# Kernel tuning notes

Hardware: AMD Instinct MI355X
Metric: run time of the kernel (lower is better)

## Reference

```python
import jax, jax.numpy as jnp
import numpy as np

B, T, F = 1024, 512, 32
H, E, L = 128, 16, 2
N_TICKERS = 5000


def _gru_layer(x_seq, W_ih, W_hh, b_ih, b_hh):
    # x_seq: [B, T, I]; W_ih: [3H, I]; W_hh: [3H, H]. PyTorch gate order: r, z, n.
    gx = jnp.einsum('bti,gi->btg', x_seq, W_ih) + b_ih  # [B, T, 3H]

    def step(h, gx_t):
        gh = h @ W_hh.T + b_hh                     # [B, 3H]
        r = jax.nn.sigmoid(gx_t[:, :H] + gh[:, :H])
        z = jax.nn.sigmoid(gx_t[:, H:2 * H] + gh[:, H:2 * H])
        n = jnp.tanh(gx_t[:, 2 * H:] + r * gh[:, 2 * H:])
        h_new = (1.0 - z) * n + z * h
        return h_new, h_new

    h0 = jnp.zeros((x_seq.shape[0], H), dtype=x_seq.dtype)
    _, hs = jax.lax.scan(step, h0, jnp.swapaxes(gx, 0, 1))  # hs: [T, B, H]
    return jnp.swapaxes(hs, 0, 1)                            # [B, T, H]


def setup_inputs() -> dict:
    key = jax.random.key(0)
    ks = jax.random.split(key, 16)
    s_in0 = 1.0 / np.sqrt(H)
    inp = {
        'x': jax.random.normal(ks[0], (B, T, F), dtype=jnp.float32),
        'ticker_ids': jax.random.randint(ks[1], (B,), 0, N_TICKERS),
        'embed': jax.random.normal(ks[2], (N_TICKERS, E), dtype=jnp.float32),
        # GRU layer 0 (input size F+E=48)
        'W_ih0': jax.random.uniform(ks[3], (3 * H, F + E), minval=-s_in0, maxval=s_in0),
        'W_hh0': jax.random.uniform(ks[4], (3 * H, H), minval=-s_in0, maxval=s_in0),
        'b_ih0': jax.random.uniform(ks[5], (3 * H,), minval=-s_in0, maxval=s_in0),
        'b_hh0': jax.random.uniform(ks[6], (3 * H,), minval=-s_in0, maxval=s_in0),
        # GRU layer 1 (input size H)
        'W_ih1': jax.random.uniform(ks[7], (3 * H, H), minval=-s_in0, maxval=s_in0),
        'W_hh1': jax.random.uniform(ks[8], (3 * H, H), minval=-s_in0, maxval=s_in0),
        'b_ih1': jax.random.uniform(ks[9], (3 * H,), minval=-s_in0, maxval=s_in0),
        'b_hh1': jax.random.uniform(ks[10], (3 * H,), minval=-s_in0, maxval=s_in0),
        # head: Linear(H,H) -> ReLU -> Linear(H,1)
        'head_w1': jax.random.uniform(ks[11], (H, H), minval=-s_in0, maxval=s_in0),
        'head_b1': jax.random.uniform(ks[12], (H,), minval=-s_in0, maxval=s_in0),
        'head_w2': jax.random.uniform(ks[13], (1, H), minval=-s_in0, maxval=s_in0),
        'head_b2': jax.random.uniform(ks[14], (1,), minval=-s_in0, maxval=s_in0),
    }
    return inp


def reference(x, ticker_ids, embed, W_ih0, W_hh0, b_ih0, b_hh0,
              W_ih1, W_hh1, b_ih1, b_hh1, head_w1, head_b1, head_w2, head_b2):
    emb = embed[ticker_ids]                                  # [B, E]
    emb_seq = jnp.broadcast_to(emb[:, None, :], (x.shape[0], x.shape[1], emb.shape[-1]))
    xcat = jnp.concatenate([x, emb_seq], axis=-1)            # [B, T, F+E]
    h = _gru_layer(xcat, W_ih0, W_hh0, b_ih0, b_hh0)         # [B, T, H]
    h = _gru_layer(h, W_ih1, W_hh1, b_ih1, b_hh1)            # [B, T, H]
    last = h[:, -1, :]                                       # [B, H]
    hid = jax.nn.relu(last @ head_w1.T + head_b1)            # dropout inactive at eval
    y = (hid @ head_w2.T + head_b2)[:, 0]                    # [B]
    return y
```

## Files before the change

### kernel.cpp

```cpp
#include <hip/hip_runtime.h>

constexpr int kB  = 1024;
constexpr int kT  = 512;
constexpr int kF  = 32;
constexpr int kE  = 16;
constexpr int kH  = 128;
constexpr int kMB = 16;
constexpr int kNMB = kB / kMB;
constexpr int kTc = 32;
constexpr int kNCh = kT / kTc;
constexpr int kTg = kTc / 2;
constexpr size_t kH0Str = (size_t)kB * kTc * kH;
constexpr size_t kSlots = (size_t)kNMB * kTc * 512;
constexpr size_t kGx0Str = kSlots * 12;

typedef __attribute__((ext_vector_type(8))) _Float16 f16x8;
typedef __attribute__((ext_vector_type(4))) _Float16 f16x4;
typedef __attribute__((ext_vector_type(4))) float    f32x4;

#define MFMA16(a,b,c) __builtin_amdgcn_mfma_f32_16x16x32_f16(a,b,c,0,0,0)

__device__ __forceinline__ float sigm_hw(float x){
    float e = __builtin_amdgcn_exp2f(-1.442695041f * x);
    return __builtin_amdgcn_rcpf(1.0f + e);
}
__device__ __forceinline__ float tanh_hw(float x){
    float e = __builtin_amdgcn_exp2f(-2.885390082f * x);
    return fmaf(2.0f, __builtin_amdgcn_rcpf(1.0f + e), -1.0f);
}
__device__ __forceinline__ void splitF(float v, _Float16 &hi, _Float16 &lo){
    hi = (_Float16)v;
    lo = (_Float16)(v - (float)hi);
}
__device__ __forceinline__ f16x8 loadW8(const float* __restrict__ p){
    f16x8 r;
#pragma unroll
    for (int j=0;j<8;j++) r[j] = (_Float16)p[j];
    return r;
}
__device__ __forceinline__ unsigned short f2u(_Float16 h){ return __builtin_bit_cast(unsigned short, h); }
__device__ __forceinline__ _Float16 u2f(unsigned short u){ return __builtin_bit_cast(_Float16, u); }
__device__ __forceinline__ unsigned pack2(float a, float b){
    return (unsigned)f2u((_Float16)a) | ((unsigned)f2u((_Float16)b) << 16);
}
__device__ __forceinline__ float uf(unsigned u){ return __builtin_bit_cast(float, u); }
__device__ __forceinline__ void bar_lds(){
    asm volatile("s_waitcnt lgkmcnt(0)\n\ts_barrier" ::: "memory");
}

struct SRec {
    alignas(16) _Float16 hH[2][16][136];
    alignas(16) _Float16 hL[2][16][136];
    alignas(16) float hf[16][132];
    alignas(16) float hf2[16][132];
};
struct SGem {
    alignas(16) _Float16 aH[2][16][136];
    alignas(16) _Float16 aL[2][16][136];
};
union SU { SRec r; SGem g; };

__attribute__((amdgpu_waves_per_eu(2, 2)))
__global__ void __launch_bounds__(512) rnn_fused(
    const float* __restrict__ x, const int* __restrict__ tick,
    const float* __restrict__ embed,
    const float* __restrict__ Wih0, const float* __restrict__ Whh0,
    const float* __restrict__ bih0, const float* __restrict__ bhh0,
    const float* __restrict__ Wih1, const float* __restrict__ bih1,
    const float* __restrict__ Whh1, const float* __restrict__ bhh1,
    const float* __restrict__ hw1, const float* __restrict__ hb1,
    const float* __restrict__ hw2, const float* __restrict__ hb2,
    unsigned* __restrict__ h0seq, unsigned* __restrict__ gxA,
    unsigned* __restrict__ gxB, float* __restrict__ h1state,
    unsigned* __restrict__ gx0, float* __restrict__ out, int c)
{
    __shared__ SU sm;
    const int tid = threadIdx.x;
    const int w = tid >> 6, l = tid & 63, lm = l & 15, lq = l >> 4;
    const int i = 16*w + lm;
    const int cls[3] = { i, 128 + i, 256 + i };

    if (blockIdx.x < 64) {
        if (c < 0 || c >= kNCh) return;
        SRec &S = sm.r;
        const int mb = blockIdx.x, b0 = mb * kMB;
        unsigned* h0w = h0seq + (size_t)(c & 1) * kH0Str;
        const unsigned* g0 = gx0 + (size_t)(c & 1) * kGx0Str;

        f16x8 wv[3][4];
#pragma unroll
        for (int T=0; T<3; T++)
#pragma unroll
            for (int kt=0; kt<4; kt++)
                wv[T][kt] = loadW8(Whh0 + (size_t)cls[T]*kH + kt*32 + lq*8);
        const float br = bhh0[cls[0]], bz = bhh0[cls[1]], bn = bhh0[cls[2]];

        float hreg[4];
        if (c == 0){
#pragma unroll
            for (int q=0;q<4;q++){
                hreg[q]=0.f;
                S.hH[0][lq*4+q][i]=(_Float16)0.f;
                S.hL[0][lq*4+q][i]=(_Float16)0.f;
            }
        } else {
            const unsigned* h0p = h0seq + (size_t)((c-1) & 1) * kH0Str;
#pragma unroll
            for (int q=0;q<4;q++){
                unsigned u = h0p[((size_t)(mb*kTc + kTc-1)*16 + lq*4+q)*kH + i];
                _Float16 hh = u2f((unsigned short)(u>>16)), hl = u2f((unsigned short)u);
                hreg[q] = (float)hh + (float)hl;
                S.hH[0][lq*4+q][i]=hh; S.hL[0][lq*4+q][i]=hl;
            }
        }
        const size_t base = (size_t)mb*kTc*512 + tid;
        uint4 grc = *(const uint4*)(g0 + base*12);
        uint4 gzc = *(const uint4*)(g0 + base*12 + 4);
        uint4 gnc = *(const uint4*)(g0 + base*12 + 8);
        uint4 grn = *(const uint4*)(g0 + (base+512)*12);
        uint4 gzn = *(const uint4*)(g0 + (base+512)*12 + 4);
        uint4 gnn = *(const uint4*)(g0 + (base+512)*12 + 8);
        bar_lds();

        int buf = 0;
        for (int tc=0; tc<kTc; tc++){
            const int nb = buf ^ 1;
            f16x8 aHf[4], aLf[4];
#pragma unroll
            for (int kt=0;kt<4;kt++){
                aHf[kt] = *(const f16x8*)&S.hH[buf][lm][kt*32 + lq*8];
                aLf[kt] = *(const f16x8*)&S.hL[buf][lm][kt*32 + lq*8];
            }
            f32x4 aR={br,br,br,br}, aZ={bz,bz,bz,bz}, aNH={bn,bn,bn,bn};
#pragma unroll
            for (int kt=0;kt<4;kt++){
                aR =MFMA16(aHf[kt],wv[0][kt],aR);  aR =MFMA16(aLf[kt],wv[0][kt],aR);
                aZ =MFMA16(aHf[kt],wv[1][kt],aZ);  aZ =MFMA16(aLf[kt],wv[1][kt],aZ);
                aNH=MFMA16(aHf[kt],wv[2][kt],aNH); aNH=MFMA16(aLf[kt],wv[2][kt],aNH);
            }
            const float rx[4] = { uf(grc.x), uf(grc.y), uf(grc.z), uf(grc.w) };
            const float zx[4] = { uf(gzc.x), uf(gzc.y), uf(gzc.z), uf(gzc.w) };
            const float nx[4] = { uf(gnc.x), uf(gnc.y), uf(gnc.z), uf(gnc.w) };
            unsigned pk[4];
#pragma unroll
            for (int q=0;q<4;q++){
                float r = sigm_hw(aR[q] + rx[q]);
                float z = sigm_hw(aZ[q] + zx[q]);
                float n = tanh_hw(fmaf(r, aNH[q], nx[q]));
                float h = fmaf(z, hreg[q]-n, n);
                hreg[q] = h;
                _Float16 hh,hl; splitF(h,hh,hl);
                S.hH[nb][lq*4+q][i]=hh;
                S.hL[nb][lq*4+q][i]=hl;
                pk[q] = ((unsigned)f2u(hh)<<16) | f2u(hl);
            }
#pragma unroll
            for (int q=0;q<4;q++)
                h0w[((size_t)(mb*kTc + tc)*16 + lq*4+q)*kH + i] = pk[q];
            grc = grn; gzc = gzn; gnc = gnn;
            int tn = tc + 2; if (tn > kTc-1) tn = kTc-1;
            grn = *(const uint4*)(g0 + (base + (size_t)tn*512)*12);
            gzn = *(const uint4*)(g0 + (base + (size_t)tn*512)*12 + 4);
            gnn = *(const uint4*)(g0 + (base + (size_t)tn*512)*12 + 8);
            bar_lds();
            buf = nb;
        }
    } else if (blockIdx.x < 192) {
        const int bid = blockIdx.x - 64;
        const int mb = bid >> 1, t0 = (bid & 1) * kTg;
        const int b0 = mb * kMB;
        const int g = c - 1;
        if (g >= 0 && g < kNCh) {
            SGem &S = sm.g;
            const unsigned* h0r = h0seq + (size_t)(g & 1) * kH0Str;
            unsigned* gA = gxA + (size_t)(g & 1) * kSlots * 4;
            unsigned* gB = gxB + (size_t)(g & 1) * kSlots * 2;

            f16x8 wv[3][4]; float bI[3];
#pragma unroll
            for (int T=0; T<3; T++){
#pragma unroll
                for (int kt=0; kt<4; kt++)
                    wv[T][kt] = loadW8(Wih1 + (size_t)cls[T]*kH + kt*32 + lq*8);
                bI[T] = bih1[cls[T]];
            }
            const int sr = tid >> 5, sq = tid & 31;
            auto ld = [&](int t){
                return *(const uint4*)(h0r + ((size_t)(mb*kTc + t)*16 + sr)*kH + 4*sq);
            };
            auto stage = [&](int bf, uint4 u){
                f16x4 vh = { u2f((unsigned short)(u.x>>16)), u2f((unsigned short)(u.y>>16)),
                             u2f((unsigned short)(u.z>>16)), u2f((unsigned short)(u.w>>16)) };
                f16x4 vl = { u2f((unsigned short)u.x), u2f((unsigned short)u.y),
                             u2f((unsigned short)u.z), u2f((unsigned short)u.w) };
                *(f16x4*)&S.aH[bf][sr][4*sq] = vh;
                *(f16x4*)&S.aL[bf][sr][4*sq] = vl;
            };
            stage(0, ld(t0));
            uint4 nxt = ld(t0 + 1);
            bar_lds();
            for (int tt=0; tt<kTg; tt++){
                const int t = t0 + tt, bf = tt & 1;
                f16x8 fH[4], fL[4];
#pragma unroll
                for (int kt=0;kt<4;kt++){
                    fH[kt] = *(const f16x8*)&S.aH[bf][lm][kt*32 + lq*8];
                    fL[kt] = *(const f16x8*)&S.aL[bf][lm][kt*32 + lq*8];
                }
                if (tt+1 < kTg) stage(bf^1, nxt);
                if (tt+2 < kTg) nxt = ld(t0 + tt + 2);
                f32x4 aR = {bI[0],bI[0],bI[0],bI[0]};
                f32x4 aZ = {bI[1],bI[1],bI[1],bI[1]};
                f32x4 aN = {bI[2],bI[2],bI[2],bI[2]};
#pragma unroll
                for (int kt=0;kt<4;kt++){
                    aR=MFMA16(fH[kt],wv[0][kt],aR); aR=MFMA16(fL[kt],wv[0][kt],aR);
                    aZ=MFMA16(fH[kt],wv[1][kt],aZ); aZ=MFMA16(fL[kt],wv[1][kt],aZ);
                    aN=MFMA16(fH[kt],wv[2][kt],aN); aN=MFMA16(fL[kt],wv[2][kt],aN);
                }
                const size_t slot = ((size_t)mb*kTc + t)*512 + tid;
                *(uint4*)(gA + slot*4) = make_uint4(pack2(aR[0],aR[1]), pack2(aR[2],aR[3]),
                                                    pack2(aZ[0],aZ[1]), pack2(aZ[2],aZ[3]));
                *(uint2*)(gB + slot*2) = make_uint2(pack2(aN[0],aN[1]), pack2(aN[2],aN[3]));
                bar_lds();
            }
        }
        const int p = c + 1;
        if (p >= 0 && p < kNCh) {
            unsigned* g0w = gx0 + (size_t)(p & 1) * kGx0Str;
            f16x8 xw[3];
#pragma unroll
            for (int T=0; T<3; T++)
                xw[T] = loadW8(Wih0 + (size_t)cls[T]*48 + lq*8);
            float ini[3][4];
            {
                const float bi0 = bih0[cls[0]], bi1 = bih0[cls[1]], bi2 = bih0[cls[2]];
                const float* w0 = Wih0 + (size_t)cls[0]*48 + 32;
                const float* w1 = Wih0 + (size_t)cls[1]*48 + 32;
                const float* w2 = Wih0 + (size_t)cls[2]*48 + 32;
#pragma unroll
                for (int q=0; q<4; q++){
                    const float* ep = embed + (size_t)tick[b0 + lq*4 + q] * kE;
                    float s0=0.f, s1=0.f, s2=0.f;
#pragma unroll
                    for (int e=0; e<kE; e++){
                        float ev = ep[e];
                        s0 = fmaf(ev, w0[e], s0);
                        s1 = fmaf(ev, w1[e], s1);
                        s2 = fmaf(ev, w2[e], s2);
                    }
                    ini[0][q]=bi0+s0; ini[1][q]=bi1+s1; ini[2][q]=bi2+s2;
                }
            }
            for (int tt=0; tt<kTg; tt++){
                const int t = t0 + tt;
                const float* xp = x + (size_t)(b0+lm)*kT*kF + (size_t)(p*kTc + t)*kF + lq*8;
                const float4 xa = *(const float4*)xp;
                const float4 xb = *(const float4*)(xp + 4);
                const float xv[8] = { xa.x, xa.y, xa.z, xa.w, xb.x, xb.y, xb.z, xb.w };
                f16x8 xH, xL;
#pragma unroll
                for (int j=0;j<8;j++){
                    _Float16 hh,hl; splitF(xv[j],hh,hl);
                    xH[j]=hh; xL[j]=hl;
                }
                f32x4 aR = {ini[0][0],ini[0][1],ini[0][2],ini[0][3]};
                f32x4 aZ = {ini[1][0],ini[1][1],ini[1][2],ini[1][3]};
                f32x4 aN = {ini[2][0],ini[2][1],ini[2][2],ini[2][3]};
                aR=MFMA16(xH,xw[0],aR); aR=MFMA16(xL,xw[0],aR);
                aZ=MFMA16(xH,xw[1],aZ); aZ=MFMA16(xL,xw[1],aZ);
                aN=MFMA16(xH,xw[2],aN); aN=MFMA16(xL,xw[2],aN);
                const size_t slot = ((size_t)mb*kTc + t)*512 + tid;
                *(uint4*)(g0w + slot*12)     = __builtin_bit_cast(uint4, aR);
                *(uint4*)(g0w + slot*12 + 4) = __builtin_bit_cast(uint4, aZ);
                *(uint4*)(g0w + slot*12 + 8) = __builtin_bit_cast(uint4, aN);
            }
        }
    } else {
        const int e0 = c - 2;
        if (e0 < 0 || e0 >= kNCh) return;
        SRec &S = sm.r;
        const int mb = blockIdx.x - 192, b0 = mb * kMB;
        const unsigned* gA = gxA + (size_t)(e0 & 1) * kSlots * 4;
        const unsigned* gB = gxB + (size_t)(e0 & 1) * kSlots * 2;

        f16x8 wv[3][4];
#pragma unroll
        for (int T=0; T<3; T++)
#pragma unroll
            for (int kt=0; kt<4; kt++)
                wv[T][kt] = loadW8(Whh1 + (size_t)cls[T]*kH + kt*32 + lq*8);
        const float br = bhh1[cls[0]], bz = bhh1[cls[1]], bn = bhh1[cls[2]];

        float hreg[4];
        if (e0 == 0){
#pragma unroll
            for (int q=0;q<4;q++){
                hreg[q]=0.f;
                S.hH[0][lq*4+q][i]=(_Float16)0.f;
                S.hL[0][lq*4+q][i]=(_Float16)0.f;
            }
        } else {
#pragma unroll
            for (int q=0;q<4;q++){
                float h = h1state[(size_t)(b0 + lq*4+q)*kH + i];
                hreg[q]=h;
                _Float16 hh,hl; splitF(h,hh,hl);
                S.hH[0][lq*4+q][i]=hh; S.hL[0][lq*4+q][i]=hl;
            }
        }
        const size_t base = (size_t)mb*kTc*512 + tid;
        uint4 g4c = *(const uint4*)(gA + base*4);
        uint2 g2c = *(const uint2*)(gB + base*2);
        uint4 g4n = *(const uint4*)(gA + (base + 512)*4);
        uint2 g2n = *(const uint2*)(gB + (base + 512)*2);
        bar_lds();

        int buf = 0;
        for (int tc=0; tc<kTc; tc++){
            const int nb = buf ^ 1;
            f16x8 aHf[4], aLf[4];
#pragma unroll
            for (int kt=0;kt<4;kt++){
                aHf[kt] = *(const f16x8*)&S.hH[buf][lm][kt*32 + lq*8];
                aLf[kt] = *(const f16x8*)&S.hL[buf][lm][kt*32 + lq*8];
            }
            f32x4 aR={br,br,br,br}, aZ={bz,bz,bz,bz}, aNH={bn,bn,bn,bn};
#pragma unroll
            for (int kt=0;kt<4;kt++){
                aR =MFMA16(aHf[kt],wv[0][kt],aR);  aR =MFMA16(aLf[kt],wv[0][kt],aR);
                aZ =MFMA16(aHf[kt],wv[1][kt],aZ);  aZ =MFMA16(aLf[kt],wv[1][kt],aZ);
                aNH=MFMA16(aHf[kt],wv[2][kt],aNH); aNH=MFMA16(aLf[kt],wv[2][kt],aNH);
            }
            const float rx[4] = { (float)u2f((unsigned short)g4c.x), (float)u2f((unsigned short)(g4c.x>>16)),
                                  (float)u2f((unsigned short)g4c.y), (float)u2f((unsigned short)(g4c.y>>16)) };
            const float zx[4] = { (float)u2f((unsigned short)g4c.z), (float)u2f((unsigned short)(g4c.z>>16)),
                                  (float)u2f((unsigned short)g4c.w), (float)u2f((unsigned short)(g4c.w>>16)) };
            const float nx[4] = { (float)u2f((unsigned short)g2c.x), (float)u2f((unsigned short)(g2c.x>>16)),
                                  (float)u2f((unsigned short)g2c.y), (float)u2f((unsigned short)(g2c.y>>16)) };
#pragma unroll
            for (int q=0;q<4;q++){
                float r = sigm_hw(aR[q] + rx[q]);
                float z = sigm_hw(aZ[q] + zx[q]);
                float n = tanh_hw(fmaf(r, aNH[q], nx[q]));
                float h = fmaf(z, hreg[q]-n, n);
                hreg[q] = h;
                _Float16 hh,hl; splitF(h,hh,hl);
                S.hH[nb][lq*4+q][i]=hh;
                S.hL[nb][lq*4+q][i]=hl;
            }
            g4c = g4n; g2c = g2n;
            int tn = tc + 2; if (tn > kTc-1) tn = kTc-1;
            g4n = *(const uint4*)(gA + (base + (size_t)tn*512)*4);
            g2n = *(const uint2*)(gB + (base + (size_t)tn*512)*2);
            bar_lds();
            buf = nb;
        }
#pragma unroll
        for (int q=0;q<4;q++)
            h1state[(size_t)(b0 + lq*4+q)*kH + i] = hreg[q];
        if (e0 == kNCh-1){
#pragma unroll
            for (int q=0;q<4;q++) S.hf[lq*4+q][i] = hreg[q];
            __syncthreads();
            const int hm = tid >> 5, i0 = (tid & 31) * 4;
#pragma unroll
            for (int e=0;e<4;e++){
                const float* wr = hw1 + (size_t)(i0+e)*kH;
                float s = hb1[i0+e];
                for (int k2=0;k2<kH;k2++) s = fmaf(wr[k2], S.hf[hm][k2], s);
                S.hf2[hm][i0+e] = fmaxf(s, 0.f);
            }
            __syncthreads();
            if (tid < kMB){
                float s = hb2[0];
                for (int k2=0;k2<kH;k2++) s = fmaf(S.hf2[tid][k2], hw2[k2], s);
                out[b0 + tid] = s;
            }
        }
    }
}

extern "C" void kernel_launch(void* const* d_in, const int* in_sizes, int n_in,
                              void* d_out, int out_size, void* d_ws, size_t ws_size,
                              hipStream_t stream)
{
    const float* x     = (const float*)d_in[0];
    const int*   tick  = (const int*)d_in[1];
    const float* embed = (const float*)d_in[2];
    const float* Wih0  = (const float*)d_in[3];
    const float* Whh0  = (const float*)d_in[4];
    const float* bih0  = (const float*)d_in[5];
    const float* bhh0  = (const float*)d_in[6];
    const float* Wih1  = (const float*)d_in[7];
    const float* Whh1  = (const float*)d_in[8];
    const float* bih1  = (const float*)d_in[9];
    const float* bhh1  = (const float*)d_in[10];
    const float* hw1   = (const float*)d_in[11];
    const float* hb1   = (const float*)d_in[12];
    const float* hw2   = (const float*)d_in[13];
    const float* hb2   = (const float*)d_in[14];
    float* out = (float*)d_out;

    unsigned* h0seq = (unsigned*)d_ws;
    unsigned* gxA   = h0seq + 2*kH0Str;
    unsigned* gxB   = gxA + 2*kSlots*4;
    float*  h1state = (float*)(gxB + 2*kSlots*2);
    unsigned* gx0   = (unsigned*)(h1state + (size_t)kB*kH);

    for (int c = -1; c <= kNCh + 1; c++){
        rnn_fused<<<256, 512, 0, stream>>>(x, tick, embed,
            Wih0, Whh0, bih0, bhh0, Wih1, bih1, Whh1, bhh1,
            hw1, hb1, hw2, hb2, h0seq, gxA, gxB, h1state, gx0, out, c);
    }
}
```

Before: 1.077 ms.

## Halve block size so each wave computes two 16-column hidden tiles

Blocks shrink from 512 to 256 threads (4 waves), and each wave now owns two 16-column slices of the hidden dimension (A and B), holding twice the weight fragments in registers and issuing twice the MFMAs per step. The A fragments read from LDS are reused across both slices, and fewer waves take part in each per-timestep barrier. This is meant to cut barrier and LDS-read overhead in the serial recurrence. In exchange it raises register pressure and per-wave serial work, and leaves fewer waves to hide latency.

```diff
diff --git a/kernel.cpp b/kernel.cpp
--- a/kernel.cpp
+++ b/kernel.cpp
@@ -60,8 +60,11 @@
 };
 union SU { SRec r; SGem g; };
 
-__attribute__((amdgpu_waves_per_eu(2, 2)))
-__global__ void __launch_bounds__(512) rnn_fused(
+struct G3 { uint4 r, z, n; };
+struct G2 { uint4 a; uint2 b; };
+
+__attribute__((amdgpu_waves_per_eu(1)))
+__global__ void __launch_bounds__(256) rnn_fused(
     const float* __restrict__ x, const int* __restrict__ tick,
     const float* __restrict__ embed,
     const float* __restrict__ Wih0, const float* __restrict__ Whh0,
@@ -77,49 +80,58 @@
     __shared__ SU sm;
     const int tid = threadIdx.x;
     const int w = tid >> 6, l = tid & 63, lm = l & 15, lq = l >> 4;
-    const int i = 16*w + lm;
-    const int cls[3] = { i, 128 + i, 256 + i };
+    const int iA = 32*w + lm, iB = iA + 16;
+    const int clsA[3] = { iA, 128 + iA, 256 + iA };
+    const int clsB[3] = { iB, 128 + iB, 256 + iB };
 
     if (blockIdx.x < 64) {
         if (c < 0 || c >= kNCh) return;
         SRec &S = sm.r;
-        const int mb = blockIdx.x, b0 = mb * kMB;
+        const int mb = blockIdx.x;
         unsigned* h0w = h0seq + (size_t)(c & 1) * kH0Str;
         const unsigned* g0 = gx0 + (size_t)(c & 1) * kGx0Str;
 
-        f16x8 wv[3][4];
+        f16x8 wvA[3][4], wvB[3][4];
 #pragma unroll
         for (int T=0; T<3; T++)
 #pragma unroll
-            for (int kt=0; kt<4; kt++)
-                wv[T][kt] = loadW8(Whh0 + (size_t)cls[T]*kH + kt*32 + lq*8);
-        const float br = bhh0[cls[0]], bz = bhh0[cls[1]], bn = bhh0[cls[2]];
-
-        float hreg[4];
+            for (int kt=0; kt<4; kt++){
+                wvA[T][kt] = loadW8(Whh0 + (size_t)clsA[T]*kH + kt*32 + lq*8);
+                wvB[T][kt] = loadW8(Whh0 + (size_t)clsB[T]*kH + kt*32 + lq*8);
+            }
+        const float brA = bhh0[clsA[0]], bzA = bhh0[clsA[1]], bnA = bhh0[clsA[2]];
+        const float brB = bhh0[clsB[0]], bzB = bhh0[clsB[1]], bnB = bhh0[clsB[2]];
+
+        float hregA[4], hregB[4];
         if (c == 0){
 #pragma unroll
             for (int q=0;q<4;q++){
-                hreg[q]=0.f;
-                S.hH[0][lq*4+q][i]=(_Float16)0.f;
-                S.hL[0][lq*4+q][i]=(_Float16)0.f;
+                hregA[q]=0.f; hregB[q]=0.f;
+                S.hH[0][lq*4+q][iA]=(_Float16)0.f; S.hL[0][lq*4+q][iA]=(_Float16)0.f;
+                S.hH[0][lq*4+q][iB]=(_Float16)0.f; S.hL[0][lq*4+q][iB]=(_Float16)0.f;
             }
         } else {
             const unsigned* h0p = h0seq + (size_t)((c-1) & 1) * kH0Str;
 #pragma unroll
             for (int q=0;q<4;q++){
-                unsigned u = h0p[((size_t)(mb*kTc + kTc-1)*16 + lq*4+q)*kH + i];
-                _Float16 hh = u2f((unsigned short)(u>>16)), hl = u2f((unsigned short)u);
-                hreg[q] = (float)hh + (float)hl;
-                S.hH[0][lq*4+q][i]=hh; S.hL[0][lq*4+q][i]=hl;
-            }
-        }
-        const size_t base = (size_t)mb*kTc*512 + tid;
-        uint4 grc = *(const uint4*)(g0 + base*12);
-        uint4 gzc = *(const uint4*)(g0 + base*12 + 4);
-        uint4 gnc = *(const uint4*)(g0 + base*12 + 8);
-        uint4 grn = *(const uint4*)(g0 + (base+512)*12);
-        uint4 gzn = *(const uint4*)(g0 + (base+512)*12 + 4);
-        uint4 gnn = *(const uint4*)(g0 + (base+512)*12 + 8);
+                unsigned uA = h0p[((size_t)(mb*kTc + kTc-1)*16 + lq*4+q)*kH + iA];
+                unsigned uB = h0p[((size_t)(mb*kTc + kTc-1)*16 + lq*4+q)*kH + iB];
+                _Float16 hhA = u2f((unsigned short)(uA>>16)), hlA = u2f((unsigned short)uA);
+                _Float16 hhB = u2f((unsigned short)(uB>>16)), hlB = u2f((unsigned short)uB);
+                hregA[q] = (float)hhA + (float)hlA;
+                hregB[q] = (float)hhB + (float)hlB;
+                S.hH[0][lq*4+q][iA]=hhA; S.hL[0][lq*4+q][iA]=hlA;
+                S.hH[0][lq*4+q][iB]=hhB; S.hL[0][lq*4+q][iB]=hlB;
+            }
+        }
+        const size_t s0 = (size_t)mb*kTc*512 + 128*w + l;
+        const size_t s1 = s0 + 64;
+        auto ld3 = [&](size_t slot){
+            G3 g; const unsigned* p = g0 + slot*12;
+            g.r = *(const uint4*)p; g.z = *(const uint4*)(p+4); g.n = *(const uint4*)(p+8);
+            return g;
+        };
+        G3 cA = ld3(s0), cB = ld3(s1), nA = ld3(s0+512), nB = ld3(s1+512);
         bar_lds();
 
         int buf = 0;
@@ -131,37 +143,55 @@
                 aHf[kt] = *(const f16x8*)&S.hH[buf][lm][kt*32 + lq*8];
                 aLf[kt] = *(const f16x8*)&S.hL[buf][lm][kt*32 + lq*8];
             }
-            f32x4 aR={br,br,br,br}, aZ={bz,bz,bz,bz}, aNH={bn,bn,bn,bn};
+            f32x4 aRA={brA,brA,brA,brA}, aZA={bzA,bzA,bzA,bzA}, aNA={bnA,bnA,bnA,bnA};
+            f32x4 aRB={brB,brB,brB,brB}, aZB={bzB,bzB,bzB,bzB}, aNB={bnB,bnB,bnB,bnB};
 #pragma unroll
             for (int kt=0;kt<4;kt++){
-                aR =MFMA16(aHf[kt],wv[0][kt],aR);  aR =MFMA16(aLf[kt],wv[0][kt],aR);
-                aZ =MFMA16(aHf[kt],wv[1][kt],aZ);  aZ =MFMA16(aLf[kt],wv[1][kt],aZ);
-                aNH=MFMA16(aHf[kt],wv[2][kt],aNH); aNH=MFMA16(aLf[kt],wv[2][kt],aNH);
-            }
-            const float rx[4] = { uf(grc.x), uf(grc.y), uf(grc.z), uf(grc.w) };
-            const float zx[4] = { uf(gzc.x), uf(gzc.y), uf(gzc.z), uf(gzc.w) };
-            const float nx[4] = { uf(gnc.x), uf(gnc.y), uf(gnc.z), uf(gnc.w) };
-            unsigned pk[4];
-#pragma unroll
-            for (int q=0;q<4;q++){
-                float r = sigm_hw(aR[q] + rx[q]);
-                float z = sigm_hw(aZ[q] + zx[q]);
-                float n = tanh_hw(fmaf(r, aNH[q], nx[q]));
-                float h = fmaf(z, hreg[q]-n, n);
-                hreg[q] = h;
+                aRA=MFMA16(aHf[kt],wvA[0][kt],aRA); aRA=MFMA16(aLf[kt],wvA[0][kt],aRA);
+                aZA=MFMA16(aHf[kt],wvA[1][kt],aZA); aZA=MFMA16(aLf[kt],wvA[1][kt],aZA);
+                aNA=MFMA16(aHf[kt],wvA[2][kt],aNA); aNA=MFMA16(aLf[kt],wvA[2][kt],aNA);
+                aRB=MFMA16(aHf[kt],wvB[0][kt],aRB); aRB=MFMA16(aLf[kt],wvB[0][kt],aRB);
+                aZB=MFMA16(aHf[kt],wvB[1][kt],aZB); aZB=MFMA16(aLf[kt],wvB[1][kt],aZB);
+                aNB=MFMA16(aHf[kt],wvB[2][kt],aNB); aNB=MFMA16(aLf[kt],wvB[2][kt],aNB);
+            }
+            unsigned pkA[4], pkB[4];
+#pragma unroll
+            for (int q=0;q<4;q++){
+                const float rxA[4] = { uf(cA.r.x), uf(cA.r.y), uf(cA.r.z), uf(cA.r.w) };
+                const float zxA[4] = { uf(cA.z.x), uf(cA.z.y), uf(cA.z.z), uf(cA.z.w) };
+                const float nxA[4] = { uf(cA.n.x), uf(cA.n.y), uf(cA.n.z), uf(cA.n.w) };
+                float r = sigm_hw(aRA[q] + rxA[q]);
+                float z = sigm_hw(aZA[q] + zxA[q]);
+                float n = tanh_hw(fmaf(r, aNA[q], nxA[q]));
+                float h = fmaf(z, hregA[q]-n, n);
+                hregA[q] = h;
                 _Float16 hh,hl; splitF(h,hh,hl);
-                S.hH[nb][lq*4+q][i]=hh;
-                S.hL[nb][lq*4+q][i]=hl;
-                pk[q] = ((unsigned)f2u(hh)<<16) | f2u(hl);
-            }
-#pragma unroll
-            for (int q=0;q<4;q++)
-                h0w[((size_t)(mb*kTc + tc)*16 + lq*4+q)*kH + i] = pk[q];
-            grc = grn; gzc = gzn; gnc = gnn;
+                S.hH[nb][lq*4+q][iA]=hh; S.hL[nb][lq*4+q][iA]=hl;
+                pkA[q] = ((unsigned)f2u(hh)<<16) | f2u(hl);
+            }
+#pragma unroll
+            for (int q=0;q<4;q++){
+                const float rxB[4] = { uf(cB.r.x), uf(cB.r.y), uf(cB.r.z), uf(cB.r.w) };
+                const float zxB[4] = { uf(cB.z.x), uf(cB.z.y), uf(cB.z.z), uf(cB.z.w) };
+                const float nxB[4] = { uf(cB.n.x), uf(cB.n.y), uf(cB.n.z), uf(cB.n.w) };
+                float r = sigm_hw(aRB[q] + rxB[q]);
+                float z = sigm_hw(aZB[q] + zxB[q]);
+                float n = tanh_hw(fmaf(r, aNB[q], nxB[q]));
+                float h = fmaf(z, hregB[q]-n, n);
+                hregB[q] = h;
+                _Float16 hh,hl; splitF(h,hh,hl);
+                S.hH[nb][lq*4+q][iB]=hh; S.hL[nb][lq*4+q][iB]=hl;
+                pkB[q] = ((unsigned)f2u(hh)<<16) | f2u(hl);
+            }
+#pragma unroll
+            for (int q=0;q<4;q++){
+                h0w[((size_t)(mb*kTc + tc)*16 + lq*4+q)*kH + iA] = pkA[q];
+                h0w[((size_t)(mb*kTc + tc)*16 + lq*4+q)*kH + iB] = pkB[q];
+            }
+            cA = nA; cB = nB;
             int tn = tc + 2; if (tn > kTc-1) tn = kTc-1;
-            grn = *(const uint4*)(g0 + (base + (size_t)tn*512)*12);
-            gzn = *(const uint4*)(g0 + (base + (size_t)tn*512)*12 + 4);
-            gnn = *(const uint4*)(g0 + (base + (size_t)tn*512)*12 + 8);
+            nA = ld3(s0 + (size_t)tn*512);
+            nB = ld3(s1 + (size_t)tn*512);
             bar_lds();
             buf = nb;
         }
@@ -176,28 +206,37 @@
             unsigned* gA = gxA + (size_t)(g & 1) * kSlots * 4;
             unsigned* gB = gxB + (size_t)(g & 1) * kSlots * 2;
 
-            f16x8 wv[3][4]; float bI[3];
+            f16x8 wvA[3][4], wvB[3][4]; float bIA[3], bIB[3];
 #pragma unroll
             for (int T=0; T<3; T++){
 #pragma unroll
-                for (int kt=0; kt<4; kt++)
-                    wv[T][kt] = loadW8(Wih1 + (size_t)cls[T]*kH + kt*32 + lq*8);
-                bI[T] = bih1[cls[T]];
-            }
-            const int sr = tid >> 5, sq = tid & 31;
-            auto ld = [&](int t){
-                return *(const uint4*)(h0r + ((size_t)(mb*kTc + t)*16 + sr)*kH + 4*sq);
+                for (int kt=0; kt<4; kt++){
+                    wvA[T][kt] = loadW8(Wih1 + (size_t)clsA[T]*kH + kt*32 + lq*8);
+                    wvB[T][kt] = loadW8(Wih1 + (size_t)clsB[T]*kH + kt*32 + lq*8);
+                }
+                bIA[T] = bih1[clsA[T]];
+                bIB[T] = bih1[clsB[T]];
+            }
+            const int sr = tid >> 4, sq = tid & 15;
+            auto ld = [&](int t, uint4 &u0, uint4 &u1){
+                const unsigned* p = h0r + ((size_t)(mb*kTc + t)*16 + sr)*kH + 8*sq;
+                u0 = *(const uint4*)p; u1 = *(const uint4*)(p+4);
             };
-            auto stage = [&](int bf, uint4 u){
-                f16x4 vh = { u2f((unsigned short)(u.x>>16)), u2f((unsigned short)(u.y>>16)),
-                             u2f((unsigned short)(u.z>>16)), u2f((unsigned short)(u.w>>16)) };
-                f16x4 vl = { u2f((unsigned short)u.x), u2f((unsigned short)u.y),
-                             u2f((unsigned short)u.z), u2f((unsigned short)u.w) };
-                *(f16x4*)&S.aH[bf][sr][4*sq] = vh;
-                *(f16x4*)&S.aL[bf][sr][4*sq] = vl;
+            auto stage = [&](int bf, uint4 u0, uint4 u1){
+                const unsigned us[8] = { u0.x,u0.y,u0.z,u0.w, u1.x,u1.y,u1.z,u1.w };
+                f16x8 vh, vl;
+#pragma unroll
+                for (int j=0;j<8;j++){
+                    vh[j] = u2f((unsigned short)(us[j]>>16));
+                    vl[j] = u2f((unsigned short)us[j]);
+                }
+                *(f16x8*)&S.aH[bf][sr][8*sq] = vh;
+                *(f16x8*)&S.aL[bf][sr][8*sq] = vl;
             };
-            stage(0, ld(t0));
-            uint4 nxt = ld(t0 + 1);
+            uint4 c0, c1, n0, n1;
+            ld(t0, c0, c1);
+            stage(0, c0, c1);
+            ld(t0 + 1, n0, n1);
             bar_lds();
             for (int tt=0; tt<kTg; tt++){
                 const int t = t0 + tt, bf = tt & 1;
@@ -207,49 +246,62 @@
                     fH[kt] = *(const f16x8*)&S.aH[bf][lm][kt*32 + lq*8];
                     fL[kt] = *(const f16x8*)&S.aL[bf][lm][kt*32 + lq*8];
                 }
-                if (tt+1 < kTg) stage(bf^1, nxt);
-                if (tt+2 < kTg) nxt = ld(t0 + tt + 2);
-                f32x4 aR = {bI[0],bI[0],bI[0],bI[0]};
-                f32x4 aZ = {bI[1],bI[1],bI[1],bI[1]};
-                f32x4 aN = {bI[2],bI[2],bI[2],bI[2]};
+                if (tt+1 < kTg) stage(bf^1, n0, n1);
+                if (tt+2 < kTg) ld(t0 + tt + 2, n0, n1);
+                f32x4 aRA = {bIA[0],bIA[0],bIA[0],bIA[0]};
+                f32x4 aZA = {bIA[1],bIA[1],bIA[1],bIA[1]};
+                f32x4 aNA = {bIA[2],bIA[2],bIA[2],bIA[2]};
+                f32x4 aRB = {bIB[0],bIB[0],bIB[0],bIB[0]};
+                f32x4 aZB = {bIB[1],bIB[1],bIB[1],bIB[1]};
+                f32x4 aNB = {bIB[2],bIB[2],bIB[2],bIB[2]};
 #pragma unroll
                 for (int kt=0;kt<4;kt++){
-                    aR=MFMA16(fH[kt],wv[0][kt],aR); aR=MFMA16(fL[kt],wv[0][kt],aR);
-                    aZ=MFMA16(fH[kt],wv[1][kt],aZ); aZ=MFMA16(fL[kt],wv[1][kt],aZ);
-                    aN=MFMA16(fH[kt],wv[2][kt],aN); aN=MFMA16(fL[kt],wv[2][kt],aN);
+                    aRA=MFMA16(fH[kt],wvA[0][kt],aRA); aRA=MFMA16(fL[kt],wvA[0][kt],aRA);
+                    aZA=MFMA16(fH[kt],wvA[1][kt],aZA); aZA=MFMA16(fL[kt],wvA[1][kt],aZA);
+                    aNA=MFMA16(fH[kt],wvA[2][kt],aNA); aNA=MFMA16(fL[kt],wvA[2][kt],aNA);
+                    aRB=MFMA16(fH[kt],wvB[0][kt],aRB); aRB=MFMA16(fL[kt],wvB[0][kt],aRB);
+                    aZB=MFMA16(fH[kt],wvB[1][kt],aZB); aZB=MFMA16(fL[kt],wvB[1][kt],aZB);
+                    aNB=MFMA16(fH[kt],wvB[2][kt],aNB); aNB=MFMA16(fL[kt],wvB[2][kt],aNB);
                 }
-                const size_t slot = ((size_t)mb*kTc + t)*512 + tid;
-                *(uint4*)(gA + slot*4) = make_uint4(pack2(aR[0],aR[1]), pack2(aR[2],aR[3]),
-                                                    pack2(aZ[0],aZ[1]), pack2(aZ[2],aZ[3]));
-                *(uint2*)(gB + slot*2) = make_uint2(pack2(aN[0],aN[1]), pack2(aN[2],aN[3]));
+                const size_t slotA = ((size_t)mb*kTc + t)*512 + 128*w + l;
+                const size_t slotB = slotA + 64;
+                *(uint4*)(gA + slotA*4) = make_uint4(pack2(aRA[0],aRA[1]), pack2(aRA[2],aRA[3]),
+                                                     pack2(aZA[0],aZA[1]), pack2(aZA[2],aZA[3]));
+                *(uint2*)(gB + slotA*2) = make_uint2(pack2(aNA[0],aNA[1]), pack2(aNA[2],aNA[3]));
+                *(uint4*)(gA + slotB*4) = make_uint4(pack2(aRB[0],aRB[1]), pack2(aRB[2],aRB[3]),
+                                                     pack2(aZB[0],aZB[1]), pack2(aZB[2],aZB[3]));
+                *(uint2*)(gB + slotB*2) = make_uint2(pack2(aNB[0],aNB[1]), pack2(aNB[2],aNB[3]));
                 bar_lds();
             }
         }
         const int p = c + 1;
         if (p >= 0 && p < kNCh) {
             unsigned* g0w = gx0 + (size_t)(p & 1) * kGx0Str;
-            f16x8 xw[3];
-#pragma unroll
-            for (int T=0; T<3; T++)
-                xw[T] = loadW8(Wih0 + (size_t)cls[T]*48 + lq*8);
-            float ini[3][4];
+            f16x8 xwA[3], xwB[3];
+#pragma unroll
+            for (int T=0; T<3; T++){
+                xwA[T] = loadW8(Wih0 + (size_t)clsA[T]*48 + lq*8);
+                xwB[T] = loadW8(Wih0 + (size_t)clsB[T]*48 + lq*8);
+            }
+            float iniA[3][4], iniB[3][4];
             {
-                const float bi0 = bih0[cls[0]], bi1 = bih0[cls[1]], bi2 = bih0[cls[2]];
-                const float* w0 = Wih0 + (size_t)cls[0]*48 + 32;
-                const float* w1 = Wih0 + (size_t)cls[1]*48 + 32;
-                const float* w2 = Wih0 + (size_t)cls[2]*48 + 32;
 #pragma unroll
                 for (int q=0; q<4; q++){
                     const float* ep = embed + (size_t)tick[b0 + lq*4 + q] * kE;
-                    float s0=0.f, s1=0.f, s2=0.f;
-#pragma unroll
-                    for (int e=0; e<kE; e++){
-                        float ev = ep[e];
-                        s0 = fmaf(ev, w0[e], s0);
-                        s1 = fmaf(ev, w1[e], s1);
-                        s2 = fmaf(ev, w2[e], s2);
+#pragma unroll
+                    for (int T=0; T<3; T++){
+                        const float* wA = Wih0 + (size_t)clsA[T]*48 + 32;
+                        const float* wB = Wih0 + (size_t)clsB[T]*48 + 32;
+                        float sA=0.f, sB=0.f;
+#pragma unroll
+                        for (int e=0; e<kE; e++){
+                            float ev = ep[e];
+                            sA = fmaf(ev, wA[e], sA);
+                            sB = fmaf(ev, wB[e], sB);
+                        }
+                        iniA[T][q] = bih0[clsA[T]] + sA;
+                        iniB[T][q] = bih0[clsB[T]] + sB;
                     }
-                    ini[0][q]=bi0+s0; ini[1][q]=bi1+s1; ini[2][q]=bi2+s2;
                 }
             }
             for (int tt=0; tt<kTg; tt++){
@@ -264,16 +316,26 @@
                     _Float16 hh,hl; splitF(xv[j],hh,hl);
                     xH[j]=hh; xL[j]=hl;
                 }
-                f32x4 aR = {ini[0][0],ini[0][1],ini[0][2],ini[0][3]};
-                f32x4 aZ = {ini[1][0],ini[1][1],ini[1][2],ini[1][3]};
-                f32x4 aN = {ini[2][0],ini[2][1],ini[2][2],ini[2][3]};
-                aR=MFMA16(xH,xw[0],aR); aR=MFMA16(xL,xw[0],aR);
-                aZ=MFMA16(xH,xw[1],aZ); aZ=MFMA16(xL,xw[1],aZ);
-                aN=MFMA16(xH,xw[2],aN); aN=MFMA16(xL,xw[2],aN);
-                const size_t slot = ((size_t)mb*kTc + t)*512 + tid;
-                *(uint4*)(g0w + slot*12)     = __builtin_bit_cast(uint4, aR);
-                *(uint4*)(g0w + slot*12 + 4) = __builtin_bit_cast(uint4, aZ);
-                *(uint4*)(g0w + slot*12 + 8) = __builtin_bit_cast(uint4, aN);
+                f32x4 aRA = {iniA[0][0],iniA[0][1],iniA[0][2],iniA[0][3]};
+                f32x4 aZA = {iniA[1][0],iniA[1][1],iniA[1][2],iniA[1][3]};
+                f32x4 aNA = {iniA[2][0],iniA[2][1],iniA[2][2],iniA[2][3]};
+                f32x4 aRB = {iniB[0][0],iniB[0][1],iniB[0][2],iniB[0][3]};
+                f32x4 aZB = {iniB[1][0],iniB[1][1],iniB[1][2],iniB[1][3]};
+                f32x4 aNB = {iniB[2][0],iniB[2][1],iniB[2][2],iniB[2][3]};
+                aRA=MFMA16(xH,xwA[0],aRA); aRA=MFMA16(xL,xwA[0],aRA);
+                aZA=MFMA16(xH,xwA[1],aZA); aZA=MFMA16(xL,xwA[1],aZA);
+                aNA=MFMA16(xH,xwA[2],aNA); aNA=MFMA16(xL,xwA[2],aNA);
+                aRB=MFMA16(xH,xwB[0],aRB); aRB=MFMA16(xL,xwB[0],aRB);
+                aZB=MFMA16(xH,xwB[1],aZB); aZB=MFMA16(xL,xwB[1],aZB);
+                aNB=MFMA16(xH,xwB[2],aNB); aNB=MFMA16(xL,xwB[2],aNB);
+                const size_t slotA = ((size_t)mb*kTc + t)*512 + 128*w + l;
+                const size_t slotB = slotA + 64;
+                *(uint4*)(g0w + slotA*12)     = __builtin_bit_cast(uint4, aRA);
+                *(uint4*)(g0w + slotA*12 + 4) = __builtin_bit_cast(uint4, aZA);
+                *(uint4*)(g0w + slotA*12 + 8) = __builtin_bit_cast(uint4, aNA);
+                *(uint4*)(g0w + slotB*12)     = __builtin_bit_cast(uint4, aRB);
+                *(uint4*)(g0w + slotB*12 + 4) = __builtin_bit_cast(uint4, aZB);
+                *(uint4*)(g0w + slotB*12 + 8) = __builtin_bit_cast(uint4, aNB);
             }
         }
     } else {
@@ -284,36 +346,45 @@
         const unsigned* gA = gxA + (size_t)(e0 & 1) * kSlots * 4;
         const unsigned* gB = gxB + (size_t)(e0 & 1) * kSlots * 2;
 
-        f16x8 wv[3][4];
+        f16x8 wvA[3][4], wvB[3][4];
 #pragma unroll
         for (int T=0; T<3; T++)
 #pragma unroll
-            for (int kt=0; kt<4; kt++)
-                wv[T][kt] = loadW8(Whh1 + (size_t)cls[T]*kH + kt*32 + lq*8);
-        const float br = bhh1[cls[0]], bz = bhh1[cls[1]], bn = bhh1[cls[2]];
-
-        float hreg[4];
+            for (int kt=0; kt<4; kt++){
+                wvA[T][kt] = loadW8(Whh1 + (size_t)clsA[T]*kH + kt*32 + lq*8);
+                wvB[T][kt] = loadW8(Whh1 + (size_t)clsB[T]*kH + kt*32 + lq*8);
+            }
+        const float brA = bhh1[clsA[0]], bzA = bhh1[clsA[1]], bnA = bhh1[clsA[2]];
+        const float brB = bhh1[clsB[0]], bzB = bhh1[clsB[1]], bnB = bhh1[clsB[2]];
+
+        float hregA[4], hregB[4];
         if (e0 == 0){
 #pragma unroll
             for (int q=0;q<4;q++){
-                hreg[q]=0.f;
-                S.hH[0][lq*4+q][i]=(_Float16)0.f;
-                S.hL[0][lq*4+q][i]=(_Float16)0.f;
+                hregA[q]=0.f; hregB[q]=0.f;
+                S.hH[0][lq*4+q][iA]=(_Float16)0.f; S.hL[0][lq*4+q][iA]=(_Float16)0.f;
+                S.hH[0][lq*4+q][iB]=(_Float16)0.f; S.hL[0][lq*4+q][iB]=(_Float16)0.f;
             }
         } else {
 #pragma unroll
             for (int q=0;q<4;q++){
-                float h = h1state[(size_t)(b0 + lq*4+q)*kH + i];
-                hreg[q]=h;
-                _Float16 hh,hl; splitF(h,hh,hl);
-                S.hH[0][lq*4+q][i]=hh; S.hL[0][lq*4+q][i]=hl;
-            }
-        }
-        const size_t base = (size_t)mb*kTc*512 + tid;
-        uint4 g4c = *(const uint4*)(gA + base*4);
-        uint2 g2c = *(const uint2*)(gB + base*2);
-        uint4 g4n = *(const uint4*)(gA + (base + 512)*4);
-        uint2 g2n = *(const uint2*)(gB + (base + 512)*2);
+                float hA = h1state[(size_t)(b0 + lq*4+q)*kH + iA];
+                float hB = h1state[(size_t)(b0 + lq*4+q)*kH + iB];
+                hregA[q]=hA; hregB[q]=hB;
+                _Float16 hh,hl;
+                splitF(hA,hh,hl); S.hH[0][lq*4+q][iA]=hh; S.hL[0][lq*4+q][iA]=hl;
+                splitF(hB,hh,hl); S.hH[0][lq*4+q][iB]=hh; S.hL[0][lq*4+q][iB]=hl;
+            }
+        }
+        const size_t s0 = (size_t)mb*kTc*512 + 128*w + l;
+        const size_t s1 = s0 + 64;
+        auto ld2 = [&](size_t slot){
+            G2 g;
+            g.a = *(const uint4*)(gA + slot*4);
+            g.b = *(const uint2*)(gB + slot*2);
+            return g;
+        };
+        G2 cA = ld2(s0), cB = ld2(s1), nA = ld2(s0+512), nB = ld2(s1+512);
         bar_lds();
 
         int buf = 0;
@@ -325,47 +396,71 @@
                 aHf[kt] = *(const f16x8*)&S.hH[buf][lm][kt*32 + lq*8];
                 aLf[kt] = *(const f16x8*)&S.hL[buf][lm][kt*32 + lq*8];
             }
-            f32x4 aR={br,br,br,br}, aZ={bz,bz,bz,bz}, aNH={bn,bn,bn,bn};
+            f32x4 aRA={brA,brA,brA,brA}, aZA={bzA,bzA,bzA,bzA}, aNA={bnA,bnA,bnA,bnA};
+            f32x4 aRB={brB,brB,brB,brB}, aZB={bzB,bzB,bzB,bzB}, aNB={bnB,bnB,bnB,bnB};
 #pragma unroll
             for (int kt=0;kt<4;kt++){
-                aR =MFMA16(aHf[kt],wv[0][kt],aR);  aR =MFMA16(aLf[kt],wv[0][kt],aR);
-                aZ =MFMA16(aHf[kt],wv[1][kt],aZ);  aZ =MFMA16(aLf[kt],wv[1][kt],aZ);
-                aNH=MFMA16(aHf[kt],wv[2][kt],aNH); aNH=MFMA16(aLf[kt],wv[2][kt],aNH);
-            }
-            const float rx[4] = { (float)u2f((unsigned short)g4c.x), (float)u2f((unsigned short)(g4c.x>>16)),
-                                  (float)u2f((unsigned short)g4c.y), (float)u2f((unsigned short)(g4c.y>>16)) };
-            const float zx[4] = { (float)u2f((unsigned short)g4c.z), (float)u2f((unsigned short)(g4c.z>>16)),
-                                  (float)u2f((unsigned short)g4c.w), (float)u2f((unsigned short)(g4c.w>>16)) };
-            const float nx[4] = { (float)u2f((unsigned short)g2c.x), (float)u2f((unsigned short)(g2c.x>>16)),
-                                  (float)u2f((unsigned short)g2c.y), (float)u2f((unsigned short)(g2c.y>>16)) };
-#pragma unroll
-            for (int q=0;q<4;q++){
-                float r = sigm_hw(aR[q] + rx[q]);
-                float z = sigm_hw(aZ[q] + zx[q]);
-                float n = tanh_hw(fmaf(r, aNH[q], nx[q]));
-                float h = fmaf(z, hreg[q]-n, n);
-                hreg[q] = h;
+                aRA=MFMA16(aHf[kt],wvA[0][kt],aRA); aRA=MFMA16(aLf[kt],wvA[0][kt],aRA);
+                aZA=MFMA16(aHf[kt],wvA[1][kt],aZA); aZA=MFMA16(aLf[kt],wvA[1][kt],aZA);
+                aNA=MFMA16(aHf[kt],wvA[2][kt],aNA); aNA=MFMA16(aLf[kt],wvA[2][kt],aNA);
+                aRB=MFMA16(aHf[kt],wvB[0][kt],aRB); aRB=MFMA16(aLf[kt],wvB[0][kt],aRB);
+                aZB=MFMA16(aHf[kt],wvB[1][kt],aZB); aZB=MFMA16(aLf[kt],wvB[1][kt],aZB);
+                aNB=MFMA16(aHf[kt],wvB[2][kt],aNB); aNB=MFMA16(aLf[kt],wvB[2][kt],aNB);
+            }
+#pragma unroll
+            for (int q=0;q<4;q++){
+                const float rx[4] = { (float)u2f((unsigned short)cA.a.x), (float)u2f((unsigned short)(cA.a.x>>16)),
+                                      (float)u2f((unsigned short)cA.a.y), (float)u2f((unsigned short)(cA.a.y>>16)) };
+                const float zx[4] = { (float)u2f((unsigned short)cA.a.z), (float)u2f((unsigned short)(cA.a.z>>16)),
+                                      (float)u2f((unsigned short)cA.a.w), (float)u2f((unsigned short)(cA.a.w>>16)) };
+                const float nx[4] = { (float)u2f((unsigned short)cA.b.x), (float)u2f((unsigned short)(cA.b.x>>16)),
+                                      (float)u2f((unsigned short)cA.b.y), (float)u2f((unsigned short)(cA.b.y>>16)) };
+                float r = sigm_hw(aRA[q] + rx[q]);
+                float z = sigm_hw(aZA[q] + zx[q]);
+                float n = tanh_hw(fmaf(r, aNA[q], nx[q]));
+                float h = fmaf(z, hregA[q]-n, n);
+                hregA[q] = h;
                 _Float16 hh,hl; splitF(h,hh,hl);
-                S.hH[nb][lq*4+q][i]=hh;
-                S.hL[nb][lq*4+q][i]=hl;
-            }
-            g4c = g4n; g2c = g2n;
+                S.hH[nb][lq*4+q][iA]=hh; S.hL[nb][lq*4+q][iA]=hl;
+            }
+#pragma unroll
+            for (int q=0;q<4;q++){
+                const float rx[4] = { (float)u2f((unsigned short)cB.a.x), (float)u2f((unsigned short)(cB.a.x>>16)),
+                                      (float)u2f((unsigned short)cB.a.y), (float)u2f((unsigned short)(cB.a.y>>16)) };
+                const float zx[4] = { (float)u2f((unsigned short)cB.a.z), (float)u2f((unsigned short)(cB.a.z>>16)),
+                                      (float)u2f((unsigned short)cB.a.w), (float)u2f((unsigned short)(cB.a.w>>16)) };
+                const float nx[4] = { (float)u2f((unsigned short)cB.b.x), (float)u2f((unsigned short)(cB.b.x>>16)),
+                                      (float)u2f((unsigned short)cB.b.y), (float)u2f((unsigned short)(cB.b.y>>16)) };
+                float r = sigm_hw(aRB[q] + rx[q]);
+                float z = sigm_hw(aZB[q] + zx[q]);
+                float n = tanh_hw(fmaf(r, aNB[q], nx[q]));
+                float h = fmaf(z, hregB[q]-n, n);
+                hregB[q] = h;
+                _Float16 hh,hl; splitF(h,hh,hl);
+                S.hH[nb][lq*4+q][iB]=hh; S.hL[nb][lq*4+q][iB]=hl;
+            }
+            cA = nA; cB = nB;
             int tn = tc + 2; if (tn > kTc-1) tn = kTc-1;
-            g4n = *(const uint4*)(gA + (base + (size_t)tn*512)*4);
-            g2n = *(const uint2*)(gB + (base + (size_t)tn*512)*2);
+            nA = ld2(s0 + (size_t)tn*512);
+            nB = ld2(s1 + (size_t)tn*512);
             bar_lds();
             buf = nb;
         }
 #pragma unroll
-        for (int q=0;q<4;q++)
-            h1state[(size_t)(b0 + lq*4+q)*kH + i] = hreg[q];
+        for (int q=0;q<4;q++){
+            h1state[(size_t)(b0 + lq*4+q)*kH + iA] = hregA[q];
+            h1state[(size_t)(b0 + lq*4+q)*kH + iB] = hregB[q];
+        }
         if (e0 == kNCh-1){
 #pragma unroll
-            for (int q=0;q<4;q++) S.hf[lq*4+q][i] = hreg[q];
+            for (int q=0;q<4;q++){
+                S.hf[lq*4+q][iA] = hregA[q];
+                S.hf[lq*4+q][iB] = hregB[q];
+            }
             __syncthreads();
-            const int hm = tid >> 5, i0 = (tid & 31) * 4;
-#pragma unroll
-            for (int e=0;e<4;e++){
+            const int hm = tid >> 4, i0 = (tid & 15) * 8;
+#pragma unroll
+            for (int e=0;e<8;e++){
                 const float* wr = hw1 + (size_t)(i0+e)*kH;
                 float s = hb1[i0+e];
                 for (int k2=0;k2<kH;k2++) s = fmaf(wr[k2], S.hf[hm][k2], s);
@@ -409,7 +504,7 @@
     unsigned* gx0   = (unsigned*)(h1state + (size_t)kB*kH);
 
     for (int c = -1; c <= kNCh + 1; c++){
-        rnn_fused<<<256, 512, 0, stream>>>(x, tick, embed,
+        rnn_fused<<<256, 256, 0, stream>>>(x, tick, embed,
             Wih0, Whh0, bih0, bhh0, Wih1, bih1, Whh1, bhh1,
             hw1, hb1, hw2, hb2, h0seq, gxA, gxB, h1state, gx0, out, c);
     }
```

Result: slower. 1.123 ms (+4.2%).

## Pack two minibatch recurrences into each 1024-thread block

Applied to the files above, without the earlier changes.

Each 1024-thread block now runs two independent 512-thread sub-blocks, each with its own shared-memory slice, and the grid is halved from 256 to 128 blocks. The goal is to put two recurrence chains on one CU so one can hide the other's latency, and to shrink the launch. The occupancy hint rises from 2 to 4 waves per EU, which halves the per-thread register budget and risks spills for the register-held weight fragments. Every block-wide barrier now ties both sub-blocks together, so they advance in lockstep, and only half as many CUs carry work.

```diff
diff --git a/kernel.cpp b/kernel.cpp
--- a/kernel.cpp
+++ b/kernel.cpp
@@ -51,17 +51,21 @@
 struct SRec {
     alignas(16) _Float16 hH[2][16][136];
     alignas(16) _Float16 hL[2][16][136];
-    alignas(16) float hf[16][132];
-    alignas(16) float hf2[16][132];
 };
 struct SGem {
     alignas(16) _Float16 aH[2][16][136];
     alignas(16) _Float16 aL[2][16][136];
 };
-union SU { SRec r; SGem g; };
-
-__attribute__((amdgpu_waves_per_eu(2, 2)))
-__global__ void __launch_bounds__(512) rnn_fused(
+struct SHead {
+    alignas(16) float hf[16][132];
+    alignas(16) float hf2[16][132];
+};
+union SU { SRec r; SGem g; SHead h; };
+
+struct G3 { uint4 r, z, n; };
+
+__attribute__((amdgpu_waves_per_eu(4, 4)))
+__global__ void __launch_bounds__(1024) rnn_fused(
     const float* __restrict__ x, const int* __restrict__ tick,
     const float* __restrict__ embed,
     const float* __restrict__ Wih0, const float* __restrict__ Whh0,
@@ -74,16 +78,17 @@
     unsigned* __restrict__ gxB, float* __restrict__ h1state,
     unsigned* __restrict__ gx0, float* __restrict__ out, int c)
 {
-    __shared__ SU sm;
+    __shared__ SU sm[2];
     const int tid = threadIdx.x;
-    const int w = tid >> 6, l = tid & 63, lm = l & 15, lq = l >> 4;
+    const int sub = tid >> 9, t5 = tid & 511;
+    const int w = t5 >> 6, l = tid & 63, lm = l & 15, lq = l >> 4;
     const int i = 16*w + lm;
     const int cls[3] = { i, 128 + i, 256 + i };
 
-    if (blockIdx.x < 64) {
+    if (blockIdx.x < 32) {
         if (c < 0 || c >= kNCh) return;
-        SRec &S = sm.r;
-        const int mb = blockIdx.x, b0 = mb * kMB;
+        SRec &S = sm[sub].r;
+        const int mb = blockIdx.x*2 + sub;
         unsigned* h0w = h0seq + (size_t)(c & 1) * kH0Str;
         const unsigned* g0 = gx0 + (size_t)(c & 1) * kGx0Str;
 
@@ -113,13 +118,13 @@
                 S.hH[0][lq*4+q][i]=hh; S.hL[0][lq*4+q][i]=hl;
             }
         }
-        const size_t base = (size_t)mb*kTc*512 + tid;
-        uint4 grc = *(const uint4*)(g0 + base*12);
-        uint4 gzc = *(const uint4*)(g0 + base*12 + 4);
-        uint4 gnc = *(const uint4*)(g0 + base*12 + 8);
-        uint4 grn = *(const uint4*)(g0 + (base+512)*12);
-        uint4 gzn = *(const uint4*)(g0 + (base+512)*12 + 4);
-        uint4 gnn = *(const uint4*)(g0 + (base+512)*12 + 8);
+        const size_t base = (size_t)mb*kTc*512 + t5;
+        auto ld3 = [&](size_t slot){
+            G3 g; const unsigned* p = g0 + slot*12;
+            g.r = *(const uint4*)p; g.z = *(const uint4*)(p+4); g.n = *(const uint4*)(p+8);
+            return g;
+        };
+        G3 gc = ld3(base), gn = ld3(base + 512);
         bar_lds();
 
         int buf = 0;
@@ -138,9 +143,9 @@
                 aZ =MFMA16(aHf[kt],wv[1][kt],aZ);  aZ =MFMA16(aLf[kt],wv[1][kt],aZ);
                 aNH=MFMA16(aHf[kt],wv[2][kt],aNH); aNH=MFMA16(aLf[kt],wv[2][kt],aNH);
             }
-            const float rx[4] = { uf(grc.x), uf(grc.y), uf(grc.z), uf(grc.w) };
-            const float zx[4] = { uf(gzc.x), uf(gzc.y), uf(gzc.z), uf(gzc.w) };
-            const float nx[4] = { uf(gnc.x), uf(gnc.y), uf(gnc.z), uf(gnc.w) };
+            const float rx[4] = { uf(gc.r.x), uf(gc.r.y), uf(gc.r.z), uf(gc.r.w) };
+            const float zx[4] = { uf(gc.z.x), uf(gc.z.y), uf(gc.z.z), uf(gc.z.w) };
+            const float nx[4] = { uf(gc.n.x), uf(gc.n.y), uf(gc.n.z), uf(gc.n.w) };
             unsigned pk[4];
 #pragma unroll
             for (int q=0;q<4;q++){
@@ -157,21 +162,19 @@
 #pragma unroll
             for (int q=0;q<4;q++)
                 h0w[((size_t)(mb*kTc + tc)*16 + lq*4+q)*kH + i] = pk[q];
-            grc = grn; gzc = gzn; gnc = gnn;
+            gc = gn;
             int tn = tc + 2; if (tn > kTc-1) tn = kTc-1;
-            grn = *(const uint4*)(g0 + (base + (size_t)tn*512)*12);
-            gzn = *(const uint4*)(g0 + (base + (size_t)tn*512)*12 + 4);
-            gnn = *(const uint4*)(g0 + (base + (size_t)tn*512)*12 + 8);
+            gn = ld3(base + (size_t)tn*512);
             bar_lds();
             buf = nb;
         }
-    } else if (blockIdx.x < 192) {
-        const int bid = blockIdx.x - 64;
-        const int mb = bid >> 1, t0 = (bid & 1) * kTg;
+    } else if (blockIdx.x < 96) {
+        const int mb = blockIdx.x - 32;
+        const int t0 = sub * kTg;
         const int b0 = mb * kMB;
         const int g = c - 1;
         if (g >= 0 && g < kNCh) {
-            SGem &S = sm.g;
+            SGem &S = sm[sub].g;
             const unsigned* h0r = h0seq + (size_t)(g & 1) * kH0Str;
             unsigned* gA = gxA + (size_t)(g & 1) * kSlots * 4;
             unsigned* gB = gxB + (size_t)(g & 1) * kSlots * 2;
@@ -184,7 +187,7 @@
                     wv[T][kt] = loadW8(Wih1 + (size_t)cls[T]*kH + kt*32 + lq*8);
                 bI[T] = bih1[cls[T]];
             }
-            const int sr = tid >> 5, sq = tid & 31;
+            const int sr = t5 >> 5, sq = t5 & 31;
             auto ld = [&](int t){
                 return *(const uint4*)(h0r + ((size_t)(mb*kTc + t)*16 + sr)*kH + 4*sq);
             };
@@ -218,7 +221,7 @@
                     aZ=MFMA16(fH[kt],wv[1][kt],aZ); aZ=MFMA16(fL[kt],wv[1][kt],aZ);
                     aN=MFMA16(fH[kt],wv[2][kt],aN); aN=MFMA16(fL[kt],wv[2][kt],aN);
                 }
-                const size_t slot = ((size_t)mb*kTc + t)*512 + tid;
+                const size_t slot = ((size_t)mb*kTc + t)*512 + t5;
                 *(uint4*)(gA + slot*4) = make_uint4(pack2(aR[0],aR[1]), pack2(aR[2],aR[3]),
                                                     pack2(aZ[0],aZ[1]), pack2(aZ[2],aZ[3]));
                 *(uint2*)(gB + slot*2) = make_uint2(pack2(aN[0],aN[1]), pack2(aN[2],aN[3]));
@@ -270,7 +273,7 @@
                 aR=MFMA16(xH,xw[0],aR); aR=MFMA16(xL,xw[0],aR);
                 aZ=MFMA16(xH,xw[1],aZ); aZ=MFMA16(xL,xw[1],aZ);
                 aN=MFMA16(xH,xw[2],aN); aN=MFMA16(xL,xw[2],aN);
-                const size_t slot = ((size_t)mb*kTc + t)*512 + tid;
+                const size_t slot = ((size_t)mb*kTc + t)*512 + t5;
                 *(uint4*)(g0w + slot*12)     = __builtin_bit_cast(uint4, aR);
                 *(uint4*)(g0w + slot*12 + 4) = __builtin_bit_cast(uint4, aZ);
                 *(uint4*)(g0w + slot*12 + 8) = __builtin_bit_cast(uint4, aN);
@@ -279,8 +282,8 @@
     } else {
         const int e0 = c - 2;
         if (e0 < 0 || e0 >= kNCh) return;
-        SRec &S = sm.r;
-        const int mb = blockIdx.x - 192, b0 = mb * kMB;
+        SRec &S = sm[sub].r;
+        const int mb = (blockIdx.x - 96)*2 + sub, b0 = mb * kMB;
         const unsigned* gA = gxA + (size_t)(e0 & 1) * kSlots * 4;
         const unsigned* gB = gxB + (size_t)(e0 & 1) * kSlots * 2;
 
@@ -309,7 +312,7 @@
                 S.hH[0][lq*4+q][i]=hh; S.hL[0][lq*4+q][i]=hl;
             }
         }
-        const size_t base = (size_t)mb*kTc*512 + tid;
+        const size_t base = (size_t)mb*kTc*512 + t5;
         uint4 g4c = *(const uint4*)(gA + base*4);
         uint2 g2c = *(const uint2*)(gB + base*2);
         uint4 g4n = *(const uint4*)(gA + (base + 512)*4);
@@ -360,22 +363,24 @@
         for (int q=0;q<4;q++)
             h1state[(size_t)(b0 + lq*4+q)*kH + i] = hreg[q];
         if (e0 == kNCh-1){
-#pragma unroll
-            for (int q=0;q<4;q++) S.hf[lq*4+q][i] = hreg[q];
+            SHead &SH = sm[sub].h;
             __syncthreads();
-            const int hm = tid >> 5, i0 = (tid & 31) * 4;
+#pragma unroll
+            for (int q=0;q<4;q++) SH.hf[lq*4+q][i] = hreg[q];
+            __syncthreads();
+            const int hm = t5 >> 5, i0 = (t5 & 31) * 4;
 #pragma unroll
             for (int e=0;e<4;e++){
                 const float* wr = hw1 + (size_t)(i0+e)*kH;
                 float s = hb1[i0+e];
-                for (int k2=0;k2<kH;k2++) s = fmaf(wr[k2], S.hf[hm][k2], s);
-                S.hf2[hm][i0+e] = fmaxf(s, 0.f);
+                for (int k2=0;k2<kH;k2++) s = fmaf(wr[k2], SH.hf[hm][k2], s);
+                SH.hf2[hm][i0+e] = fmaxf(s, 0.f);
             }
             __syncthreads();
-            if (tid < kMB){
+            if (t5 < kMB){
                 float s = hb2[0];
-                for (int k2=0;k2<kH;k2++) s = fmaf(S.hf2[tid][k2], hw2[k2], s);
-                out[b0 + tid] = s;
+                for (int k2=0;k2<kH;k2++) s = fmaf(SH.hf2[t5][k2], hw2[k2], s);
+                out[b0 + t5] = s;
             }
         }
     }
@@ -409,7 +414,7 @@
     unsigned* gx0   = (unsigned*)(h1state + (size_t)kB*kH);
 
     for (int c = -1; c <= kNCh + 1; c++){
-        rnn_fused<<<256, 512, 0, stream>>>(x, tick, embed,
+        rnn_fused<<<128, 1024, 0, stream>>>(x, tick, embed,
             Wih0, Whh0, bih0, bhh0, Wih1, bih1, Whh1, bhh1,
             hw1, hb1, hw2, hb2, h0seq, gxA, gxB, h1state, gx0, out, c);
     }
```

Result: slower. 1.832 ms (+70.1%).
